# Performance work log

Hardware: AMD Instinct MI355X
Metric: run time of the kernel (lower is better)

The kernel has to match this reference:

```python
import jax, jax.numpy as jnp
import numpy as np

EMBED = 256
HEADS = 8
HEAD_DIM = EMBED // HEADS
K = 7          # kernel_size
DIL = 1        # dilation
PAD = DIL * (K - 1) // 2  # 3
B, H, W = 4, 56, 56


def setup_inputs() -> dict:
    key = jax.random.key(0)
    ks = jax.random.split(key, 9)
    d = {"x": jax.random.normal(ks[0], (B, H, W, EMBED), jnp.float32)}
    for i, name in enumerate(["wq", "wk", "wv", "wo"]):
        d[name] = jax.random.normal(ks[1 + i], (EMBED, EMBED), jnp.float32) * 0.02
    for i, name in enumerate(["bq", "bk", "bv", "bo"]):
        d[name] = jax.random.normal(ks[5 + i], (EMBED,), jnp.float32) * 0.02
    return d


def _unfold(t):
    # t: [N, d, H, W] -> [N, d, K*K, H, W]; zero padding (matches F.unfold),
    # so out-of-bounds neighbors contribute logit 0, NOT -inf (faithful to source).
    h, w = t.shape[2], t.shape[3]
    tp = jnp.pad(t, ((0, 0), (0, 0), (PAD, PAD), (PAD, PAD)))
    patches = [tp[:, :, i * DIL:i * DIL + h, j * DIL:j * DIL + w]
               for i in range(K) for j in range(K)]  # fixed K*K=49 offsets
    return jnp.stack(patches, axis=2)


def reference(x, wq, bq, wk, bk, wv, bv, wo, bo):
    b, h, w, c = x.shape
    scale = HEAD_DIM ** -0.5
    q = x @ wq.T + bq
    k = x @ wk.T + bk
    v = x @ wv.T + bv

    def to_nh(t):  # [B,H,W,C] -> [B*heads, head_dim, H, W]
        return t.reshape(b, h, w, HEADS, HEAD_DIM).transpose(0, 3, 4, 1, 2).reshape(b * HEADS, HEAD_DIM, h, w)

    q, k, v = to_nh(q), to_nh(k), to_nh(v)
    k_unf = _unfold(k)  # [N, d, K2, H, W]
    v_unf = _unfold(v)
    logits = jnp.einsum('ndhw,ndkhw->nkhw', q, k_unf) * scale  # [N, K2, H, W]
    attn = jax.nn.softmax(logits, axis=1)
    out = jnp.einsum('nkhw,ndkhw->ndhw', attn, v_unf)  # [N, d, H, W]
    out = out.reshape(b, HEADS, HEAD_DIM, h, w).transpose(0, 3, 4, 1, 2).reshape(b, h, w, c)
    return out @ wo.T + bo
```

## Files before the change

### kernel.cpp

```cpp
#include <hip/hip_runtime.h>

typedef unsigned int u32;
typedef unsigned short u16;
typedef __attribute__((ext_vector_type(8))) short bf16x8;
typedef __attribute__((ext_vector_type(4))) float f32x4;

#define T_TOK 12544
#define EMB   256
#define IMG   56
#define SCALE 0.17677669529663689f
#define HALO  196
#define KSTR  40
#define VTSTR 224
#define PSTR  232

__device__ __forceinline__ u32 bf16_rtne(float f) {
    u32 u = __builtin_bit_cast(u32, f);
    return (u + 0x7fffu + ((u >> 16) & 1u)) >> 16;
}
__device__ __forceinline__ float bf16_to_f(u32 h) { return __builtin_bit_cast(float, h << 16); }

#define GLD16(g, l) __builtin_amdgcn_global_load_lds( \
    (const __attribute__((address_space(1))) u32*)(g), \
    (__attribute__((address_space(3))) u32*)(l), 16, 0, 0)

__global__ __launch_bounds__(256) void convert_kernel(
    const float* __restrict__ x, const float* __restrict__ wq, const float* __restrict__ wk,
    const float* __restrict__ wv, const float* __restrict__ wo,
    u16* __restrict__ xb, u16* __restrict__ bsh,
    u16* __restrict__ boh, u16* __restrict__ bol) {
    const int i = blockIdx.x * 256 + threadIdx.x;
    const int NX4 = T_TOK * EMB / 4;
    if (i < NX4) {
        const float4 f = ((const float4*)x)[i];
        const float vf[4] = {f.x, f.y, f.z, f.w};
        ushort4 hv;
        u16* hp = (u16*)&hv;
        #pragma unroll
        for (int c = 0; c < 4; ++c) hp[c] = (u16)bf16_rtne(vf[c]);
        ((ushort4*)xb)[i] = hv;
    } else {
        const int j = i - NX4;
        const int w = j >> 14, widx = j & 16383;
        const float* src = (w == 0) ? wq : (w == 1) ? wk : (w == 2) ? wv : wo;
        const float4 f = ((const float4*)src)[widx];
        const float vf[4] = {f.x, f.y, f.z, f.w};
        if (w < 3) {
            ushort4 hv;
            u16* hp = (u16*)&hv;
            #pragma unroll
            for (int c = 0; c < 4; ++c) hp[c] = (u16)bf16_rtne(vf[c]);
            ((ushort4*)bsh)[(w << 14) + widx] = hv;
        } else {
            ushort4 hv, lv;
            u16* hp = (u16*)&hv; u16* lp = (u16*)&lv;
            #pragma unroll
            for (int c = 0; c < 4; ++c) {
                const u32 h = bf16_rtne(vf[c]);
                hp[c] = (u16)h;
                lp[c] = (u16)bf16_rtne(vf[c] - bf16_to_f(h));
            }
            ((ushort4*)boh)[widx] = hv;
            ((ushort4*)bol)[widx] = lv;
        }
    }
}

__global__ __launch_bounds__(256) void qkv_mfma(
    const u16* __restrict__ xb, const u16* __restrict__ bsh,
    const float* __restrict__ bq, const float* __restrict__ bk, const float* __restrict__ bv,
    u16* __restrict__ qb, u16* __restrict__ kb, u16* __restrict__ vb) {
    __shared__ __attribute__((aligned(16))) u16 sA[2][128 * 32];
    __shared__ __attribute__((aligned(16))) u16 sB[2][128 * 32];
    const int nBase = blockIdx.x * 128;
    const int mBase = blockIdx.y * 128;
    const int tid = threadIdx.x, wv2 = tid >> 6, ln = tid & 63;
    const int lrow = ln & 15, lqd = ln >> 4;
    const int wm = (wv2 & 1) * 64, wn = (wv2 >> 1) * 64;
    const int c0 = wv2 * 128 + ln, r0 = c0 >> 2, kc0 = c0 & 3;
    const int c1 = c0 + 64,        r1 = c1 >> 2, kc1 = c1 & 3;
    const size_t gA0 = (size_t)(mBase + r0) * EMB + kc0 * 8;
    const size_t gA1 = (size_t)(mBase + r1) * EMB + kc1 * 8;
    const size_t gB0 = (size_t)(nBase + r0) * EMB + kc0 * 8;
    const size_t gB1 = (size_t)(nBase + r1) * EMB + kc1 * 8;
    const int l0 = (wv2 * 128) * 8, l1 = (wv2 * 128 + 64) * 8;

    f32x4 acc[4][4];
    #pragma unroll
    for (int mi = 0; mi < 4; ++mi)
        #pragma unroll
        for (int ni = 0; ni < 4; ++ni)
            acc[mi][ni] = (f32x4){0.f, 0.f, 0.f, 0.f};

    GLD16(xb  + gA0, &sA[0][l0]);
    GLD16(xb  + gA1, &sA[0][l1]);
    GLD16(bsh + gB0, &sB[0][l0]);
    GLD16(bsh + gB1, &sB[0][l1]);

    for (int kt = 0; kt < 8; ++kt) {
        const int b = kt & 1;
        __syncthreads();
        if (kt < 7) {
            const int k0 = (kt + 1) * 32;
            GLD16(xb  + gA0 + k0, &sA[b ^ 1][l0]);
            GLD16(xb  + gA1 + k0, &sA[b ^ 1][l1]);
            GLD16(bsh + gB0 + k0, &sB[b ^ 1][l0]);
            GLD16(bsh + gB1 + k0, &sB[b ^ 1][l1]);
        }
        bf16x8 af[4], bf[4];
        #pragma unroll
        for (int mi = 0; mi < 4; ++mi)
            af[mi] = *(const bf16x8*)&sA[b][(wm + mi * 16 + lrow) * 32 + lqd * 8];
        #pragma unroll
        for (int ni = 0; ni < 4; ++ni)
            bf[ni] = *(const bf16x8*)&sB[b][(wn + ni * 16 + lrow) * 32 + lqd * 8];
        #pragma unroll
        for (int mi = 0; mi < 4; ++mi)
            #pragma unroll
            for (int ni = 0; ni < 4; ++ni)
                acc[mi][ni] = __builtin_amdgcn_mfma_f32_16x16x32_bf16(af[mi], bf[ni], acc[mi][ni], 0, 0, 0);
    }

    const int which = nBase >> 8;
    const float* bias = (which == 0) ? bq : (which == 1) ? bk : bv;
    u16* dst = (which == 0) ? qb : (which == 1) ? kb : vb;
    #pragma unroll
    for (int ni = 0; ni < 4; ++ni) {
        const int ncol = nBase + wn + ni * 16 + lrow;
        const int c = ncol & 255;
        const float bz = bias[c];
        #pragma unroll
        for (int mi = 0; mi < 4; ++mi) {
            #pragma unroll
            for (int r = 0; r < 4; ++r) {
                const int row = mBase + wm + mi * 16 + lqd * 4 + r;
                dst[(size_t)row * EMB + c] = (u16)bf16_rtne(acc[mi][ni][r] + bz);
            }
        }
    }
}

__global__ __launch_bounds__(256) void out_mfma(
    const u16* __restrict__ aoh, const u16* __restrict__ aol,
    const u16* __restrict__ boh, const u16* __restrict__ bol,
    const float* __restrict__ bo, float* __restrict__ out) {
    __shared__ __attribute__((aligned(16))) u16 sAh[2][64 * 32];
    __shared__ __attribute__((aligned(16))) u16 sAl[2][64 * 32];
    __shared__ __attribute__((aligned(16))) u16 sBh[2][64 * 32];
    __shared__ __attribute__((aligned(16))) u16 sBl[2][64 * 32];
    const int nBase = blockIdx.x * 64;
    const int mBase = blockIdx.y * 64;
    const int tid = threadIdx.x, wv = tid >> 6, ln = tid & 63;
    const int lrow = ln & 15, lqd = ln >> 4;
    const int rA = tid >> 2, kcA = tid & 3;
    const size_t gA = (size_t)(mBase + rA) * EMB + kcA * 8;
    const size_t gB = (size_t)(nBase + rA) * EMB + kcA * 8;
    const int lA = wv * 64 * 8;

    f32x4 acc[4];
    #pragma unroll
    for (int mi = 0; mi < 4; ++mi) acc[mi] = (f32x4){0.f, 0.f, 0.f, 0.f};

    GLD16(aoh + gA, &sAh[0][lA]);
    GLD16(aol + gA, &sAl[0][lA]);
    GLD16(boh + gB, &sBh[0][lA]);
    GLD16(bol + gB, &sBl[0][lA]);

    for (int kt = 0; kt < 8; ++kt) {
        const int b = kt & 1;
        __syncthreads();
        if (kt < 7) {
            const int k0 = (kt + 1) * 32;
            GLD16(aoh + gA + k0, &sAh[b ^ 1][lA]);
            GLD16(aol + gA + k0, &sAl[b ^ 1][lA]);
            GLD16(boh + gB + k0, &sBh[b ^ 1][lA]);
            GLD16(bol + gB + k0, &sBl[b ^ 1][lA]);
        }
        bf16x8 ah[4], al[4];
        #pragma unroll
        for (int mi = 0; mi < 4; ++mi) {
            ah[mi] = *(const bf16x8*)&sAh[b][(mi * 16 + lrow) * 32 + lqd * 8];
            al[mi] = *(const bf16x8*)&sAl[b][(mi * 16 + lrow) * 32 + lqd * 8];
        }
        const bf16x8 bh = *(const bf16x8*)&sBh[b][(wv * 16 + lrow) * 32 + lqd * 8];
        const bf16x8 bl = *(const bf16x8*)&sBl[b][(wv * 16 + lrow) * 32 + lqd * 8];
        #pragma unroll
        for (int mi = 0; mi < 4; ++mi) {
            acc[mi] = __builtin_amdgcn_mfma_f32_16x16x32_bf16(ah[mi], bh, acc[mi], 0, 0, 0);
            acc[mi] = __builtin_amdgcn_mfma_f32_16x16x32_bf16(al[mi], bh, acc[mi], 0, 0, 0);
            acc[mi] = __builtin_amdgcn_mfma_f32_16x16x32_bf16(ah[mi], bl, acc[mi], 0, 0, 0);
        }
    }

    const int ncol = nBase + wv * 16 + lrow;
    const float bz = bo[ncol];
    #pragma unroll
    for (int mi = 0; mi < 4; ++mi) {
        #pragma unroll
        for (int r = 0; r < 4; ++r) {
            const int row = mBase + mi * 16 + lqd * 4 + r;
            out[(size_t)row * EMB + ncol] = acc[mi][r] + bz;
        }
    }
}

__global__ __launch_bounds__(256, 3) void attn_kernel(
    const u16* __restrict__ qb, const u16* __restrict__ kb, const u16* __restrict__ vb,
    u16* __restrict__ aoh, u16* __restrict__ aol) {
    __shared__ __attribute__((aligned(16))) u16 smem[22016];
    u16* sVT = smem;
    u16* sK  = smem + 7168;
    u16* sP  = smem + 7168;

    const int tid = threadIdx.x;
    const int w = tid >> 6, ln = tid & 63;
    const int lrow = ln & 15, lqd = ln >> 4;
    const int img = blockIdx.z >> 3, head = blockIdx.z & 7;
    const int ty0 = blockIdx.y * 8, tx0 = blockIdx.x * 8;

    for (int i = tid; i < 1792; i += 256) {
        const int mv = (i >= 896) ? 1 : 0;
        const int ii = i - 896 * mv;
        const int p = ii >> 2, c = ii & 3;
        const int pyh = p / 14, pxh = p - pyh * 14;
        const int gy = ty0 - 3 + pyh, gx = tx0 - 3 + pxh;
        const bool ok = (p < HALO) & ((unsigned)gy < 56u) & ((unsigned)gx < 56u);
        if (!mv) {
            u16* dstk = sK + p * KSTR + c * 8;
            if (ok) {
                const size_t tt = ((size_t)img * IMG + gy) * IMG + gx;
                *(uint4*)dstk = *(const uint4*)(kb + tt * EMB + head * 32 + c * 8);
            } else {
                *(uint4*)dstk = (uint4){0u, 0u, 0u, 0u};
            }
        } else {
            u16* dv = sVT + (c * 8) * VTSTR + p;
            if (ok) {
                const size_t tt = ((size_t)img * IMG + gy) * IMG + gx;
                const uint4 u = *(const uint4*)(vb + tt * EMB + head * 32 + c * 8);
                dv[0 * VTSTR] = (u16)(u.x & 0xffffu);
                dv[1 * VTSTR] = (u16)(u.x >> 16);
                dv[2 * VTSTR] = (u16)(u.y & 0xffffu);
                dv[3 * VTSTR] = (u16)(u.y >> 16);
                dv[4 * VTSTR] = (u16)(u.z & 0xffffu);
                dv[5 * VTSTR] = (u16)(u.z >> 16);
                dv[6 * VTSTR] = (u16)(u.w & 0xffffu);
                dv[7 * VTSTR] = (u16)(u.w >> 16);
            } else {
                #pragma unroll
                for (int j = 0; j < 8; ++j) dv[j * VTSTR] = 0;
            }
        }
    }

    const int mpix = w * 16 + lrow;
    const int qpy = mpix >> 3, qpx = mpix & 7;
    const size_t qtok = ((size_t)img * IMG + ty0 + qpy) * IMG + tx0 + qpx;
    const bf16x8 aq = *(const bf16x8*)&qb[qtok * EMB + head * 32 + lqd * 8];
    __syncthreads();

    f32x4 ct[13];
    #pragma unroll
    for (int t = 0; t < 13; ++t) ct[t] = (f32x4){0.f, 0.f, 0.f, 0.f};
    #pragma unroll
    for (int t = 0; t < 13; ++t) {
        const bf16x8 bk = *(const bf16x8*)&sK[(t * 16 + lrow) * KSTR + lqd * 8];
        ct[t] = __builtin_amdgcn_mfma_f32_16x16x32_bf16(aq, bk, ct[t], 0, 0, 0);
    }

    int pys[4], pxs[4];
    #pragma unroll
    for (int r = 0; r < 4; ++r) {
        const int row = lqd * 4 + r;
        pys[r] = 2 * w + (row >> 3);
        pxs[r] = row & 7;
    }
    float mr4[4] = {-1e30f, -1e30f, -1e30f, -1e30f};
    #pragma unroll
    for (int t = 0; t < 13; ++t) {
        const int col = t * 16 + lrow;
        const int hy = col / 14, hx = col - 14 * hy;
        const bool okc = (col < HALO);
        #pragma unroll
        for (int r = 0; r < 4; ++r) {
            const bool ok = ((unsigned)(hy - pys[r]) < 7u) &
                            ((unsigned)(hx - pxs[r]) < 7u) & okc;
            const float lv = ok ? ct[t][r] * SCALE : -1e30f;
            ct[t][r] = lv;
            mr4[r] = fmaxf(mr4[r], lv);
        }
    }
    #pragma unroll
    for (int r = 0; r < 4; ++r) {
        float m = mr4[r];
        m = fmaxf(m, __shfl_xor(m, 1));
        m = fmaxf(m, __shfl_xor(m, 2));
        m = fmaxf(m, __shfl_xor(m, 4));
        m = fmaxf(m, __shfl_xor(m, 8));
        mr4[r] = m;
    }
    float sr4[4] = {0.f, 0.f, 0.f, 0.f};
    #pragma unroll
    for (int t = 0; t < 13; ++t)
        #pragma unroll
        for (int r = 0; r < 4; ++r) {
            const float e = __expf(ct[t][r] - mr4[r]);
            ct[t][r] = e;
            sr4[r] += e;
        }
    #pragma unroll
    for (int r = 0; r < 4; ++r) {
        float s = sr4[r];
        s += __shfl_xor(s, 1);
        s += __shfl_xor(s, 2);
        s += __shfl_xor(s, 4);
        s += __shfl_xor(s, 8);
        sr4[r] = 1.0f / s;
    }

    __syncthreads();

    u16* sPw = sP + w * 16 * PSTR;
    #pragma unroll
    for (int t = 0; t < 13; ++t)
        #pragma unroll
        for (int r = 0; r < 4; ++r)
            sPw[(lqd * 4 + r) * PSTR + t * 16 + lrow] = (u16)bf16_rtne(ct[t][r]);
    #pragma unroll
    for (int z = 0; z < 4; ++z) {
        const int idx = z * 64 + ln;
        sPw[(idx >> 4) * PSTR + 208 + (idx & 15)] = 0;
    }

    f32x4 o0 = (f32x4){0.f, 0.f, 0.f, 0.f};
    f32x4 o1 = (f32x4){0.f, 0.f, 0.f, 0.f};
    #pragma unroll
    for (int ks = 0; ks < 7; ++ks) {
        const bf16x8 ap  = *(const bf16x8*)&sPw[lrow * PSTR + ks * 32 + lqd * 8];
        const bf16x8 bv0 = *(const bf16x8*)&sVT[lrow * VTSTR + ks * 32 + lqd * 8];
        const bf16x8 bv1 = *(const bf16x8*)&sVT[(16 + lrow) * VTSTR + ks * 32 + lqd * 8];
        o0 = __builtin_amdgcn_mfma_f32_16x16x32_bf16(ap, bv0, o0, 0, 0, 0);
        o1 = __builtin_amdgcn_mfma_f32_16x16x32_bf16(ap, bv1, o1, 0, 0, 0);
    }

    #pragma unroll
    for (int r = 0; r < 4; ++r) {
        const int row = lqd * 4 + r;
        const int opy = 2 * w + (row >> 3), opx = row & 7;
        const size_t ot = ((size_t)img * IMG + ty0 + opy) * IMG + tx0 + opx;
        const float inv = sr4[r];
        const float v0 = o0[r] * inv;
        const float v1 = o1[r] * inv;
        const size_t base = ot * EMB + head * 32;
        const u32 h0 = bf16_rtne(v0);
        aoh[base + lrow] = (u16)h0;
        aol[base + lrow] = (u16)bf16_rtne(v0 - bf16_to_f(h0));
        const u32 h1 = bf16_rtne(v1);
        aoh[base + 16 + lrow] = (u16)h1;
        aol[base + 16 + lrow] = (u16)bf16_rtne(v1 - bf16_to_f(h1));
    }
}

extern "C" void kernel_launch(void* const* d_in, const int* in_sizes, int n_in,
                              void* d_out, int out_size, void* d_ws, size_t ws_size,
                              hipStream_t stream) {
    const float* x  = (const float*)d_in[0];
    const float* wq = (const float*)d_in[1];
    const float* wk = (const float*)d_in[2];
    const float* wv = (const float*)d_in[3];
    const float* wo = (const float*)d_in[4];
    const float* bq = (const float*)d_in[5];
    const float* bk = (const float*)d_in[6];
    const float* bv = (const float*)d_in[7];
    const float* bo = (const float*)d_in[8];
    float* out = (float*)d_out;

    char* ws = (char*)d_ws;
    u16* xb  = (u16*)(ws);
    u16* qb  = (u16*)(ws +  6422528);
    u16* kb  = (u16*)(ws + 12845056);
    u16* vb  = (u16*)(ws + 19267584);
    u16* aoh = (u16*)(ws + 25690112);
    u16* aol = (u16*)(ws + 32112640);
    u16* bsh = (u16*)(ws + 38535168);
    u16* boh = (u16*)(ws + 38928384);
    u16* bol = (u16*)(ws + 39059456);

    convert_kernel<<<3392, 256, 0, stream>>>(x, wq, wk, wv, wo, xb, bsh, boh, bol);
    qkv_mfma<<<dim3(6, 98), 256, 0, stream>>>(xb, bsh, bq, bk, bv, qb, kb, vb);
    attn_kernel<<<dim3(7, 7, 32), 256, 0, stream>>>(qb, kb, vb, aoh, aol);
    out_mfma<<<dim3(4, 196), 256, 0, stream>>>(aoh, aol, boh, bol, bo, out);
}
```

Baseline: 134.0 us.

## Shrink QKV GEMM tiles to 64x64 and trim attention LDS for higher occupancy

The QKV projection GEMM moves from 128x128 tiles, where each wave computed a 64x64 sub-tile, to 64x64 tiles, where each wave computes 64x16. The grid grows from 588 to 2352 blocks, which gives more parallelism across CUs at the cost of less operand reuse per block. The attention kernel narrows its V-transpose and P strides from 224/232 to 208 and drops the zero-padded tail. The final K-step uses a half-width fragment with the upper lanes zeroed instead of a padded full step. The smaller LDS footprint lets launch bounds ask for 4 blocks per CU, at the price of extra register pressure and possible LDS bank conflicts at stride 208.

```diff
diff --git a/kernel.cpp b/kernel.cpp
--- a/kernel.cpp
+++ b/kernel.cpp
@@ -11,8 +11,8 @@
 #define SCALE 0.17677669529663689f
 #define HALO  196
 #define KSTR  40
-#define VTSTR 224
-#define PSTR  232
+#define VTSTR 208
+#define PSTR  208
 
 __device__ __forceinline__ u32 bf16_rtne(float f) {
     u32 u = __builtin_bit_cast(u32, f);
@@ -23,6 +23,12 @@
 #define GLD16(g, l) __builtin_amdgcn_global_load_lds( \
     (const __attribute__((address_space(1))) u32*)(g), \
     (__attribute__((address_space(3))) u32*)(l), 16, 0, 0)
+
+__device__ __forceinline__ bf16x8 half_frag(const u16* p) {
+    const uint2 v = *(const uint2*)p;
+    u32 tmp[4] = {v.x, v.y, 0u, 0u};
+    return *(bf16x8*)tmp;
+}
 
 __global__ __launch_bounds__(256) void convert_kernel(
     const float* __restrict__ x, const float* __restrict__ wq, const float* __restrict__ wk,
@@ -70,72 +76,53 @@
     const u16* __restrict__ xb, const u16* __restrict__ bsh,
     const float* __restrict__ bq, const float* __restrict__ bk, const float* __restrict__ bv,
     u16* __restrict__ qb, u16* __restrict__ kb, u16* __restrict__ vb) {
-    __shared__ __attribute__((aligned(16))) u16 sA[2][128 * 32];
-    __shared__ __attribute__((aligned(16))) u16 sB[2][128 * 32];
-    const int nBase = blockIdx.x * 128;
-    const int mBase = blockIdx.y * 128;
-    const int tid = threadIdx.x, wv2 = tid >> 6, ln = tid & 63;
+    __shared__ __attribute__((aligned(16))) u16 sA[2][64 * 32];
+    __shared__ __attribute__((aligned(16))) u16 sB[2][64 * 32];
+    const int nBase = blockIdx.x * 64;
+    const int mBase = blockIdx.y * 64;
+    const int tid = threadIdx.x, wv = tid >> 6, ln = tid & 63;
     const int lrow = ln & 15, lqd = ln >> 4;
-    const int wm = (wv2 & 1) * 64, wn = (wv2 >> 1) * 64;
-    const int c0 = wv2 * 128 + ln, r0 = c0 >> 2, kc0 = c0 & 3;
-    const int c1 = c0 + 64,        r1 = c1 >> 2, kc1 = c1 & 3;
-    const size_t gA0 = (size_t)(mBase + r0) * EMB + kc0 * 8;
-    const size_t gA1 = (size_t)(mBase + r1) * EMB + kc1 * 8;
-    const size_t gB0 = (size_t)(nBase + r0) * EMB + kc0 * 8;
-    const size_t gB1 = (size_t)(nBase + r1) * EMB + kc1 * 8;
-    const int l0 = (wv2 * 128) * 8, l1 = (wv2 * 128 + 64) * 8;
-
-    f32x4 acc[4][4];
-    #pragma unroll
-    for (int mi = 0; mi < 4; ++mi)
-        #pragma unroll
-        for (int ni = 0; ni < 4; ++ni)
-            acc[mi][ni] = (f32x4){0.f, 0.f, 0.f, 0.f};
-
-    GLD16(xb  + gA0, &sA[0][l0]);
-    GLD16(xb  + gA1, &sA[0][l1]);
-    GLD16(bsh + gB0, &sB[0][l0]);
-    GLD16(bsh + gB1, &sB[0][l1]);
+    const int rA = tid >> 2, kcA = tid & 3;
+    const size_t gA = (size_t)(mBase + rA) * EMB + kcA * 8;
+    const size_t gB = (size_t)(nBase + rA) * EMB + kcA * 8;
+    const int lA = wv * 64 * 8;
+
+    f32x4 acc[4];
+    #pragma unroll
+    for (int mi = 0; mi < 4; ++mi) acc[mi] = (f32x4){0.f, 0.f, 0.f, 0.f};
+
+    GLD16(xb  + gA, &sA[0][lA]);
+    GLD16(bsh + gB, &sB[0][lA]);
 
     for (int kt = 0; kt < 8; ++kt) {
         const int b = kt & 1;
         __syncthreads();
         if (kt < 7) {
             const int k0 = (kt + 1) * 32;
-            GLD16(xb  + gA0 + k0, &sA[b ^ 1][l0]);
-            GLD16(xb  + gA1 + k0, &sA[b ^ 1][l1]);
-            GLD16(bsh + gB0 + k0, &sB[b ^ 1][l0]);
-            GLD16(bsh + gB1 + k0, &sB[b ^ 1][l1]);
-        }
-        bf16x8 af[4], bf[4];
+            GLD16(xb  + gA + k0, &sA[b ^ 1][lA]);
+            GLD16(bsh + gB + k0, &sB[b ^ 1][lA]);
+        }
+        bf16x8 af[4];
         #pragma unroll
         for (int mi = 0; mi < 4; ++mi)
-            af[mi] = *(const bf16x8*)&sA[b][(wm + mi * 16 + lrow) * 32 + lqd * 8];
-        #pragma unroll
-        for (int ni = 0; ni < 4; ++ni)
-            bf[ni] = *(const bf16x8*)&sB[b][(wn + ni * 16 + lrow) * 32 + lqd * 8];
+            af[mi] = *(const bf16x8*)&sA[b][(mi * 16 + lrow) * 32 + lqd * 8];
+        const bf16x8 bf = *(const bf16x8*)&sB[b][(wv * 16 + lrow) * 32 + lqd * 8];
         #pragma unroll
         for (int mi = 0; mi < 4; ++mi)
-            #pragma unroll
-            for (int ni = 0; ni < 4; ++ni)
-                acc[mi][ni] = __builtin_amdgcn_mfma_f32_16x16x32_bf16(af[mi], bf[ni], acc[mi][ni], 0, 0, 0);
+            acc[mi] = __builtin_amdgcn_mfma_f32_16x16x32_bf16(af[mi], bf, acc[mi], 0, 0, 0);
     }
 
     const int which = nBase >> 8;
     const float* bias = (which == 0) ? bq : (which == 1) ? bk : bv;
     u16* dst = (which == 0) ? qb : (which == 1) ? kb : vb;
-    #pragma unroll
-    for (int ni = 0; ni < 4; ++ni) {
-        const int ncol = nBase + wn + ni * 16 + lrow;
-        const int c = ncol & 255;
-        const float bz = bias[c];
-        #pragma unroll
-        for (int mi = 0; mi < 4; ++mi) {
-            #pragma unroll
-            for (int r = 0; r < 4; ++r) {
-                const int row = mBase + wm + mi * 16 + lqd * 4 + r;
-                dst[(size_t)row * EMB + c] = (u16)bf16_rtne(acc[mi][ni][r] + bz);
-            }
+    const int c = (nBase & 255) + wv * 16 + lrow;
+    const float bz = bias[c];
+    #pragma unroll
+    for (int mi = 0; mi < 4; ++mi) {
+        #pragma unroll
+        for (int r = 0; r < 4; ++r) {
+            const int row = mBase + mi * 16 + lqd * 4 + r;
+            dst[(size_t)row * EMB + c] = (u16)bf16_rtne(acc[mi][r] + bz);
         }
     }
 }
@@ -204,13 +191,13 @@
     }
 }
 
-__global__ __launch_bounds__(256, 3) void attn_kernel(
+__global__ __launch_bounds__(256, 4) void attn_kernel(
     const u16* __restrict__ qb, const u16* __restrict__ kb, const u16* __restrict__ vb,
     u16* __restrict__ aoh, u16* __restrict__ aol) {
-    __shared__ __attribute__((aligned(16))) u16 smem[22016];
+    __shared__ __attribute__((aligned(16))) u16 smem[19968];
     u16* sVT = smem;
-    u16* sK  = smem + 7168;
-    u16* sP  = smem + 7168;
+    u16* sK  = smem + 6656;
+    u16* sP  = smem + 6656;
 
     const int tid = threadIdx.x;
     const int w = tid >> 6, ln = tid & 63;
@@ -218,9 +205,9 @@
     const int img = blockIdx.z >> 3, head = blockIdx.z & 7;
     const int ty0 = blockIdx.y * 8, tx0 = blockIdx.x * 8;
 
-    for (int i = tid; i < 1792; i += 256) {
-        const int mv = (i >= 896) ? 1 : 0;
-        const int ii = i - 896 * mv;
+    for (int i = tid; i < 1664; i += 256) {
+        const int mv = (i >= 832) ? 1 : 0;
+        const int ii = i - 832 * mv;
         const int p = ii >> 2, c = ii & 3;
         const int pyh = p / 14, pxh = p - pyh * 14;
         const int gy = ty0 - 3 + pyh, gx = tx0 - 3 + pxh;
@@ -326,19 +313,21 @@
         #pragma unroll
         for (int r = 0; r < 4; ++r)
             sPw[(lqd * 4 + r) * PSTR + t * 16 + lrow] = (u16)bf16_rtne(ct[t][r]);
-    #pragma unroll
-    for (int z = 0; z < 4; ++z) {
-        const int idx = z * 64 + ln;
-        sPw[(idx >> 4) * PSTR + 208 + (idx & 15)] = 0;
-    }
 
     f32x4 o0 = (f32x4){0.f, 0.f, 0.f, 0.f};
     f32x4 o1 = (f32x4){0.f, 0.f, 0.f, 0.f};
     #pragma unroll
-    for (int ks = 0; ks < 7; ++ks) {
+    for (int ks = 0; ks < 6; ++ks) {
         const bf16x8 ap  = *(const bf16x8*)&sPw[lrow * PSTR + ks * 32 + lqd * 8];
         const bf16x8 bv0 = *(const bf16x8*)&sVT[lrow * VTSTR + ks * 32 + lqd * 8];
         const bf16x8 bv1 = *(const bf16x8*)&sVT[(16 + lrow) * VTSTR + ks * 32 + lqd * 8];
+        o0 = __builtin_amdgcn_mfma_f32_16x16x32_bf16(ap, bv0, o0, 0, 0, 0);
+        o1 = __builtin_amdgcn_mfma_f32_16x16x32_bf16(ap, bv1, o1, 0, 0, 0);
+    }
+    {
+        const bf16x8 ap  = half_frag(&sPw[lrow * PSTR + 192 + lqd * 4]);
+        const bf16x8 bv0 = half_frag(&sVT[lrow * VTSTR + 192 + lqd * 4]);
+        const bf16x8 bv1 = half_frag(&sVT[(16 + lrow) * VTSTR + 192 + lqd * 4]);
         o0 = __builtin_amdgcn_mfma_f32_16x16x32_bf16(ap, bv0, o0, 0, 0, 0);
         o1 = __builtin_amdgcn_mfma_f32_16x16x32_bf16(ap, bv1, o1, 0, 0, 0);
     }
@@ -387,7 +376,7 @@
     u16* bol = (u16*)(ws + 39059456);
 
     convert_kernel<<<3392, 256, 0, stream>>>(x, wq, wk, wv, wo, xb, bsh, boh, bol);
-    qkv_mfma<<<dim3(6, 98), 256, 0, stream>>>(xb, bsh, bq, bk, bv, qb, kb, vb);
+    qkv_mfma<<<dim3(12, 196), 256, 0, stream>>>(xb, bsh, bq, bk, bv, qb, kb, vb);
     attn_kernel<<<dim3(7, 7, 32), 256, 0, stream>>>(qb, kb, vb, aoh, aol);
     out_mfma<<<dim3(4, 196), 256, 0, stream>>>(aoh, aol, boh, bol, bo, out);
 }
```

New measurement: 134.7 us. About the same (+0.5%).
